# Kernel optimization log

Measured on AMD Instinct MI355X. Metric: run time of the kernel, lower is better.

## Reference

```python
import jax, jax.numpy as jnp
import numpy as np

B, LC, LQ = 16, 512, 64
H = 256            # args.hidden_dim (BiLSTM output dim)
D = 4 * H          # feedforward / biaffine input dim
DFF = 512          # args.hidden_dim_ffw
C = 3              # num_labels


def setup_inputs() -> dict:
    key = jax.random.key(0)
    ks = jax.random.split(key, 12)
    sc = 0.02
    return {
        "ctx_emb": jax.random.normal(ks[0], (B, LC, H), jnp.float32),
        "ques_emb": jax.random.normal(ks[1], (B, LQ, H), jnp.float32),
        "w_sim": jax.random.normal(ks[2], (3 * H,), jnp.float32) * sc,
        "W1s": jax.random.normal(ks[3], (D, DFF), jnp.float32) * sc,
        "b1s": jnp.zeros((DFF,), jnp.float32),
        "W2s": jax.random.normal(ks[4], (DFF, D), jnp.float32) * sc,
        "b2s": jnp.zeros((D,), jnp.float32),
        "W1e": jax.random.normal(ks[5], (D, DFF), jnp.float32) * sc,
        "b1e": jnp.zeros((DFF,), jnp.float32),
        "W2e": jax.random.normal(ks[6], (DFF, D), jnp.float32) * sc,
        "b2e": jnp.zeros((D,), jnp.float32),
        "Wb": jax.random.normal(ks[7], (D + 1, C, D + 1), jnp.float32) * sc,
    }


def _ffw(x, W1, b1, W2, b2):
    # FeedforwardLayer: w_2(relu(w_1(x))) (dropout is identity at eval)
    return jnp.maximum(x @ W1 + b1, 0.0) @ W2 + b2


def reference(ctx_emb, ques_emb, w_sim, W1s, b1s, W2s, b2s, W1e, b1e, W2e, b2e, Wb):
    w1, w2, w3 = jnp.split(w_sim, 3)
    # Fused BiDAF trilinear similarity: identical math to
    # Linear(cat([ctx_, ques_, ctx_*ques_], -1)) with weight [w1|w2|w3].
    sim = (ctx_emb @ w1)[:, :, None] + (ques_emb @ w2)[:, None, :] \
        + jnp.einsum('bih,bjh->bij', ctx_emb * w3, ques_emb)      # [B,LC,LQ]
    a = jax.nn.softmax(sim, axis=-1)                               # [B,LC,LQ]
    c2q = jnp.einsum('bij,bjh->bih', a, ques_emb)                  # [B,LC,H]
    b = jax.nn.softmax(jnp.max(sim, axis=2), axis=-1)              # [B,LC]
    q2c = jnp.einsum('bi,bih->bh', b, ctx_emb)[:, None, :]         # [B,1,H] broadcast over LC
    x = jnp.concatenate([ctx_emb, c2q, ctx_emb * c2q, ctx_emb * q2c], axis=2)  # [B,LC,4H]
    start = _ffw(x, W1s, b1s, W2s, b2s)                            # [B,LC,D]
    end = _ffw(x, W1e, b1e, W2e, b2e)                              # [B,LC,D]
    ones = jnp.ones(start.shape[:-1] + (1,), start.dtype)
    s1 = jnp.concatenate([start, ones], axis=-1)                   # [B,LC,D+1]
    e1 = jnp.concatenate([end, ones], axis=-1)                     # [B,LC,D+1]
    # Biaffine: score[b,x,y,c] = s1[b,x] . Wb[:,c,:] . e1[b,y]
    return jnp.einsum('bxi,icj,byj->bxyc', s1, Wb, e1)             # [B,LC,LC,C]
```

## Files before the change

kernel.cpp:

```cpp
#include <hip/hip_runtime.h>
#include <hip/hip_bf16.h>
#include <math.h>

typedef __bf16 bf16_t;
typedef bf16_t bf16x4 __attribute__((ext_vector_type(4)));
typedef bf16_t bf16x8 __attribute__((ext_vector_type(8)));
typedef float f32x4 __attribute__((ext_vector_type(4)));

#define Bsz 16
#define LCc 512
#define LQq 64
#define Hd 256
#define Dd 1024
#define DFFd 512
#define DP1 1025
#define KP 1152
#define NTT 18
#define NROW 8192
#define YC 1536

#define OFF_T    0L
#define OFF_QW2  0L
#define OFF_MROW 4096L
#define OFF_Q2C  36864L
#define OFF_C2Q  53248L
#define OFF_XB   8441856L
#define OFF_HBUF 25219072L
#define OFF_W1C  41996288L
#define OFF_W2C  44093440L
#define OFF_S1   56623104L
#define OFF_E1   75497472L
#define OFF_WBT  94371840L

static __device__ __forceinline__ void gload_lds16(const void* g, void* l) {
    __builtin_amdgcn_global_load_lds(
        (const __attribute__((address_space(1))) void*)g,
        (__attribute__((address_space(3))) void*)l, 16, 0, 0);
}

__global__ __launch_bounds__(256) void k_qw2(const float* __restrict__ ques,
                                             const float* __restrict__ wsim,
                                             float* __restrict__ qw2) {
    int row = blockIdx.x * 4 + (threadIdx.x >> 6);
    int lane = threadIdx.x & 63;
    float4 q = *(const float4*)&ques[(long)row * Hd + lane * 4];
    float4 w = *(const float4*)&wsim[Hd + lane * 4];
    float p = q.x * w.x + q.y * w.y + q.z * w.z + q.w * w.w;
#pragma unroll
    for (int o = 32; o >= 1; o >>= 1) p += __shfl_xor(p, o, 64);
    if (lane == 0) qw2[row] = p;
}

__global__ __launch_bounds__(256) void k_wtrans(const float* __restrict__ in,
                                                bf16_t* __restrict__ out,
                                                int K, int N) {
    __shared__ float tile[32][33];
    int k0 = blockIdx.x * 32, n0 = blockIdx.y * 32;
    int r = threadIdx.x >> 5, c = threadIdx.x & 31;
#pragma unroll
    for (int rr = 0; rr < 32; rr += 8)
        tile[r + rr][c] = in[(long)(k0 + r + rr) * N + n0 + c];
    __syncthreads();
#pragma unroll
    for (int rr = 0; rr < 32; rr += 8)
        out[(long)(n0 + r + rr) * K + k0 + c] = (bf16_t)tile[c][r + rr];
}

__global__ __launch_bounds__(256) void k_wb(const float* __restrict__ Wb,
                                            bf16_t* __restrict__ Wbt) {
    int rw = blockIdx.x;
    int c = rw >> 10, i = rw & 1023;
    int tid = threadIdx.x;
    const float* src = Wb + ((long)i * 3 + c) * DP1;
    bf16_t* orow = Wbt + (long)rw * KP;
#pragma unroll
    for (int p = 0; p < 2; p++) {
        int j4 = tid + p * 256;
        if (j4 < KP / 4) {
            int j = j4 * 4;
            float x = (j + 0 < DP1) ? src[j + 0] : 0.f;
            float y = (j + 1 < DP1) ? src[j + 1] : 0.f;
            float z = (j + 2 < DP1) ? src[j + 2] : 0.f;
            float w = (j + 3 < DP1) ? src[j + 3] : 0.f;
            bf16x4 bv = {(bf16_t)x, (bf16_t)y, (bf16_t)z, (bf16_t)w};
            *(bf16x4*)&orow[j] = bv;
        }
    }
}

__global__ __launch_bounds__(256) void k_initse(bf16_t* __restrict__ s1,
                                                bf16_t* __restrict__ e1) {
    int idx = blockIdx.x * 256 + threadIdx.x;
    long r = idx >> 7; int cc = idx & 127;
    bf16_t v = (bf16_t)(cc == 0 ? 1.0f : 0.0f);
    s1[r * KP + 1024 + cc] = v;
    e1[r * KP + 1024 + cc] = v;
}

__global__ __launch_bounds__(256) void k_attn(const float* __restrict__ ctx,
                                              const float* __restrict__ ques,
                                              const float* __restrict__ wsim,
                                              const float* __restrict__ qw2,
                                              float* __restrict__ c2q,
                                              float* __restrict__ mrow) {
    __shared__ bf16x4 qlds[LQq * 64];
    __shared__ float cw3s[4][Hd];
    __shared__ float awave[4][LQq];
    int b = blockIdx.x >> 5;
    int itile = blockIdx.x & 31;
    int tid = threadIdx.x, wid = tid >> 6, lane = tid & 63;
#pragma unroll
    for (int p = 0; p < 16; p++) {
        int s = tid + p * 256;
        int j = s >> 6, h4s = s & 63;
        int h4 = h4s ^ (j & 15);
        float4 v = *(const float4*)&ques[((long)b * LQq + j) * Hd + h4 * 4];
        bf16x4 bv = {(bf16_t)v.x, (bf16_t)v.y, (bf16_t)v.z, (bf16_t)v.w};
        qlds[s] = bv;
    }
    float qw2r = qw2[b * LQq + lane];
    float4 w1v = *(const float4*)&wsim[lane * 4];
    float4 w3v = *(const float4*)&wsim[2 * Hd + lane * 4];
    __syncthreads();
    for (int rr = 0; rr < 4; rr++) {
        int i = itile * 16 + wid * 4 + rr;
        float4 cv = *(const float4*)&ctx[((long)b * LCc + i) * Hd + lane * 4];
        float cw1p = cv.x * w1v.x + cv.y * w1v.y + cv.z * w1v.z + cv.w * w1v.w;
        float4 c3;
        c3.x = cv.x * w3v.x; c3.y = cv.y * w3v.y;
        c3.z = cv.z * w3v.z; c3.w = cv.w * w3v.w;
        *(float4*)&cw3s[wid][lane * 4] = c3;
#pragma unroll
        for (int o = 32; o >= 1; o >>= 1) cw1p += __shfl_xor(cw1p, o, 64);
        __syncthreads();
        float s = cw1p + qw2r;
#pragma unroll 8
        for (int h4 = 0; h4 < 64; h4++) {
            float4 c3v = *(const float4*)&cw3s[wid][h4 * 4];
            bf16x4 qb = qlds[lane * 64 + (h4 ^ (lane & 15))];
            s += c3v.x * (float)qb[0] + c3v.y * (float)qb[1]
               + c3v.z * (float)qb[2] + c3v.w * (float)qb[3];
        }
        float mx = s;
#pragma unroll
        for (int o = 32; o >= 1; o >>= 1) mx = fmaxf(mx, __shfl_xor(mx, o, 64));
        if (lane == 0) mrow[b * LCc + i] = mx;
        float pe = __expf(s - mx);
        float den = pe;
#pragma unroll
        for (int o = 32; o >= 1; o >>= 1) den += __shfl_xor(den, o, 64);
        awave[wid][lane] = pe / den;
        __syncthreads();
        float4 accv = {0.f, 0.f, 0.f, 0.f};
#pragma unroll 8
        for (int j = 0; j < 64; j++) {
            float aj = awave[wid][j];
            bf16x4 qb = qlds[j * 64 + (lane ^ (j & 15))];
            accv.x = fmaf(aj, (float)qb[0], accv.x);
            accv.y = fmaf(aj, (float)qb[1], accv.y);
            accv.z = fmaf(aj, (float)qb[2], accv.z);
            accv.w = fmaf(aj, (float)qb[3], accv.w);
        }
        *(float4*)&c2q[((long)b * LCc + i) * Hd + lane * 4] = accv;
        __syncthreads();
    }
}

__global__ __launch_bounds__(256) void k_q2c(const float* __restrict__ ctx,
                                             const float* __restrict__ mrow,
                                             float* __restrict__ q2c) {
    __shared__ float wbuf[LCc];
    __shared__ float red[8];
    __shared__ float part[8][32];
    int blk = blockIdx.x;
    int b = blk >> 3, hc = blk & 7;
    int tid = threadIdx.x;
    float v0 = mrow[b * LCc + tid], v1 = mrow[b * LCc + 256 + tid];
    float m = fmaxf(v0, v1);
#pragma unroll
    for (int o = 32; o >= 1; o >>= 1) m = fmaxf(m, __shfl_xor(m, o, 64));
    if ((tid & 63) == 0) red[tid >> 6] = m;
    __syncthreads();
    float M = fmaxf(fmaxf(red[0], red[1]), fmaxf(red[2], red[3]));
    float e0 = __expf(v0 - M), e1v = __expf(v1 - M);
    float sm = e0 + e1v;
#pragma unroll
    for (int o = 32; o >= 1; o >>= 1) sm += __shfl_xor(sm, o, 64);
    if ((tid & 63) == 0) red[4 + (tid >> 6)] = sm;
    __syncthreads();
    float S = red[4] + red[5] + red[6] + red[7];
    wbuf[tid] = e0 / S;
    wbuf[tid + 256] = e1v / S;
    __syncthreads();
    int ig = tid >> 5, h31 = tid & 31;
    int h = hc * 32 + h31;
    float acc = 0.f;
#pragma unroll 4
    for (int ii = 0; ii < 64; ii++) {
        int i = ig * 64 + ii;
        acc = fmaf(wbuf[i], ctx[((long)b * LCc + i) * Hd + h], acc);
    }
    part[ig][h31] = acc;
    __syncthreads();
    if (tid < 32) {
        float s = 0.f;
#pragma unroll
        for (int k = 0; k < 8; k++) s += part[k][tid];
        q2c[b * Hd + hc * 32 + tid] = s;
    }
}

__global__ __launch_bounds__(256) void k_buildx(const float* __restrict__ ctx,
                                                const float* __restrict__ c2q,
                                                const float* __restrict__ q2c,
                                                bf16_t* __restrict__ xb) {
    long r = blockIdx.x;
    int b = (int)(r >> 9);
    int tid = threadIdx.x;
    int sec = tid >> 6, h4 = tid & 63;
    float4 cv = *(const float4*)&ctx[r * Hd + h4 * 4];
    float4 v;
    if (sec == 0) {
        v = cv;
    } else if (sec == 1) {
        v = *(const float4*)&c2q[r * Hd + h4 * 4];
    } else if (sec == 2) {
        float4 q = *(const float4*)&c2q[r * Hd + h4 * 4];
        v.x = cv.x * q.x; v.y = cv.y * q.y; v.z = cv.z * q.z; v.w = cv.w * q.w;
    } else {
        float4 q = *(const float4*)&q2c[b * Hd + h4 * 4];
        v.x = cv.x * q.x; v.y = cv.y * q.y; v.z = cv.z * q.z; v.w = cv.w * q.w;
    }
    bf16x4 bv = {(bf16_t)v.x, (bf16_t)v.y, (bf16_t)v.z, (bf16_t)v.w};
    *(bf16x4*)&xb[r * Dd + sec * Hd + h4 * 4] = bv;
}

__global__ __launch_bounds__(256) void k_gcol(const bf16_t* __restrict__ e1,
                                              const float* __restrict__ Wb,
                                              bf16_t* __restrict__ T) {
    int tid = threadIdx.x;
    int wv = tid >> 6, lane = tid & 63;
    long r = (long)blockIdx.x * 4 + wv;
    bf16x8 ea = *(const bf16x8*)&e1[r * KP + lane * 16];
    bf16x8 eb = *(const bf16x8*)&e1[r * KP + lane * 16 + 8];
    const float* wr0 = Wb + (long)3072 * DP1;
#pragma unroll
    for (int c = 0; c < 3; c++) {
        const float* wr = wr0 + (long)c * DP1 + lane * 16;
        float acc = 0.f;
#pragma unroll
        for (int k = 0; k < 8; k++) {
            acc = fmaf((float)ea[k], wr[k], acc);
            acc = fmaf((float)eb[k], wr[8 + k], acc);
        }
#pragma unroll
        for (int o = 32; o >= 1; o >>= 1) acc += __shfl_xor(acc, o, 64);
        long rowb = (r * 3 + c) * (long)KP;
        if (lane == 0)
            T[rowb + 1024] = (bf16_t)(acc + wr0[(long)c * DP1 + 1024]);
        for (int jj = 1025 + lane; jj < KP; jj += 64)
            T[rowb + jj] = (bf16_t)0.f;
    }
}

template <int MODE>
__global__ __launch_bounds__(256, 2) void gemm_nt(
    const bf16_t* __restrict__ A, const bf16_t* __restrict__ B,
    const float* __restrict__ bias0, const float* __restrict__ bias1,
    bf16_t* __restrict__ C0, bf16_t* __restrict__ C1) {
    const int K = (MODE == 0) ? 1024 : 512;
    const int lda = 1024;
    const int ldb = (MODE == 0) ? 1024 : 512;
    __shared__ bf16_t As[128 * 32];
    __shared__ bf16_t Bs[128 * 32];
    int tid = threadIdx.x;
    int wid = tid >> 6, lane = tid & 63;
    int z = (MODE == 1) ? blockIdx.z : 0;
    const bf16_t* Ab = A + (long)blockIdx.x * 128 * lda + z * 512;
    const bf16_t* Bb = B + (long)z * 1024 * 512 + (long)blockIdx.y * 128 * ldb;
    int wr = (wid >> 1) * 64, wc = (wid & 1) * 64;
    int fr = lane & 15, kg = lane >> 4;
    f32x4 acc[4][4] = {};
    for (int k0 = 0; k0 < K; k0 += 32) {
        __syncthreads();
#pragma unroll
        for (int p = 0; p < 2; p++) {
            int q = tid + p * 256;
            int row = q >> 2, cg = q & 3;
            gload_lds16(Ab + (long)row * lda + k0 + cg * 8, &As[q * 8]);
            gload_lds16(Bb + (long)row * ldb + k0 + cg * 8, &Bs[q * 8]);
        }
        __syncthreads();
        bf16x8 af[4], bq[4];
#pragma unroll
        for (int m = 0; m < 4; m++)
            af[m] = *(const bf16x8*)&As[(wr + m * 16 + fr) * 32 + kg * 8];
#pragma unroll
        for (int n = 0; n < 4; n++)
            bq[n] = *(const bf16x8*)&Bs[(wc + n * 16 + fr) * 32 + kg * 8];
#pragma unroll
        for (int m = 0; m < 4; m++)
#pragma unroll
            for (int n = 0; n < 4; n++)
                acc[m][n] = __builtin_amdgcn_mfma_f32_16x16x32_bf16(
                    af[m], bq[n], acc[m][n], 0, 0, 0);
    }
    int g4 = (lane >> 4) * 4;
#pragma unroll
    for (int m = 0; m < 4; m++) {
#pragma unroll
        for (int g = 0; g < 4; g++) {
            long r = (long)blockIdx.x * 128 + wr + m * 16 + g4 + g;
#pragma unroll
            for (int n = 0; n < 4; n++) {
                int col = blockIdx.y * 128 + wc + n * 16 + fr;
                float v = acc[m][n][g];
                if (MODE == 0) {
                    v += (col < 512) ? bias0[col] : bias1[col - 512];
                    v = fmaxf(v, 0.f);
                    C0[r * 1024 + col] = (bf16_t)v;
                } else {
                    v += z ? bias1[col] : bias0[col];
                    (z ? C1 : C0)[r * (long)KP + col] = (bf16_t)v;
                }
            }
        }
    }
}

template <int MODE>
__global__ __launch_bounds__(512) void gemm8(
    const bf16_t* __restrict__ A, const bf16_t* __restrict__ B,
    void* __restrict__ C) {
    __shared__ char smem[131072];
    int tid = threadIdx.x;
    int wg = blockIdx.x;
    int bx, zz, yy;
    if (MODE == 2) {
        int wgid = (wg & 7) * 48 + (wg >> 3);
        int wi = wgid & 15, st = wgid >> 4;
        bx = (st & 7) * 4 + (wi & 3);
        int byN = (st >> 3) * 4 + (wi >> 2);
        zz = byN >> 2; yy = byN & 3;
    } else {
        int wgid = (wg & 7) * 24 + (wg >> 3);
        bx = wgid & 1;
        int byz = wgid >> 1;
        zz = byz / 6; yy = byz % 6;
    }
    long Aoff = (MODE == 2) ? (long)bx * 256 * KP
                            : ((long)zz * 512 + bx * 256) * KP;
    long Boff = (MODE == 2) ? (long)(zz * 4 + yy) * 256 * KP
                            : ((long)zz * 1536 + yy * 256) * KP;
    const bf16_t* At = A + Aoff;
    const bf16_t* Bt = B + Boff;
    int lane = tid & 63, wv = tid >> 6, wm = wv >> 2, wn = wv & 3;
    int fr = lane & 15, kg = lane >> 4;
    int row0 = tid >> 3, sc0 = (tid & 7) ^ (row0 & 7);
    int q1 = tid + 512;
    int row1 = q1 >> 3, sc1 = (q1 & 7) ^ (row1 & 7);

    auto STAGE = [&](int mat, int ht, int tile) {
        int ts = tile <= NTT - 1 ? tile : NTT - 1;
        int buf = tile & 1;
        const bf16_t* base = mat ? Bt : At;
        long rb = (long)ht * 128;
        const bf16_t* g0 = base + (rb + row0) * KP + ts * 64 + sc0 * 8;
        const bf16_t* g1 = base + (rb + row1) * KP + ts * 64 + sc1 * 8;
        char* l = smem + (mat ? 65536 : 0) + buf * 32768 + ht * 16384;
        gload_lds16(g0, l + tid * 16);
        gload_lds16(g1, l + 8192 + tid * 16);
    };
    auto RDA = [&](int buf, int h, int m, int kk) -> bf16x8 {
        int row = wm * 128 + h * 64 + m * 16 + fr;
        int c16 = kk * 4 + kg;
        int off = buf * 32768 + row * 128 + ((c16 ^ (row & 7)) << 4);
        return *(const bf16x8*)(smem + off);
    };
    auto RDB = [&](int buf, int v, int n, int kk) -> bf16x8 {
        int row = wn * 64 + v * 32 + n * 16 + fr;
        int c16 = kk * 4 + kg;
        int off = 65536 + buf * 32768 + row * 128 + ((c16 ^ (row & 7)) << 4);
        return *(const bf16x8*)(smem + off);
    };

    f32x4 acc[8][4] = {};

    STAGE(0, 0, 0); STAGE(0, 1, 0); STAGE(1, 0, 0); STAGE(1, 1, 0);
    STAGE(0, 0, 1); STAGE(0, 1, 1);
    asm volatile("s_waitcnt vmcnt(4)" ::: "memory");
    __builtin_amdgcn_s_barrier();

    auto doTile = [&](int buf, int sB, int sA) {
        bf16x8 aL[4][2], aH[4][2], bE[2][2], bO[2][2];
#pragma unroll
        for (int m = 0; m < 4; m++)
#pragma unroll
            for (int k = 0; k < 2; k++) aL[m][k] = RDA(buf, 0, m, k);
#pragma unroll
        for (int n = 0; n < 2; n++)
#pragma unroll
            for (int k = 0; k < 2; k++) bE[n][k] = RDB(buf, 0, n, k);
        STAGE(1, 0, sB);
        __builtin_amdgcn_s_barrier();
        __builtin_amdgcn_s_setprio(1);
#pragma unroll
        for (int m = 0; m < 4; m++)
#pragma unroll
            for (int n = 0; n < 2; n++)
#pragma unroll
                for (int k = 0; k < 2; k++)
                    acc[m][n] = __builtin_amdgcn_mfma_f32_16x16x32_bf16(
                        aL[m][k], bE[n][k], acc[m][n], 0, 0, 0);
        __builtin_amdgcn_s_setprio(0);
        __builtin_amdgcn_s_barrier();
#pragma unroll
        for (int n = 0; n < 2; n++)
#pragma unroll
            for (int k = 0; k < 2; k++) bO[n][k] = RDB(buf, 1, n, k);
        STAGE(1, 1, sB);
        __builtin_amdgcn_s_barrier();
        __builtin_amdgcn_s_setprio(1);
#pragma unroll
        for (int m = 0; m < 4; m++)
#pragma unroll
            for (int n = 0; n < 2; n++)
#pragma unroll
                for (int k = 0; k < 2; k++)
                    acc[m][2 + n] = __builtin_amdgcn_mfma_f32_16x16x32_bf16(
                        aL[m][k], bO[n][k], acc[m][2 + n], 0, 0, 0);
        __builtin_amdgcn_s_setprio(0);
        __builtin_amdgcn_s_barrier();
#pragma unroll
        for (int m = 0; m < 4; m++)
#pragma unroll
            for (int k = 0; k < 2; k++) aH[m][k] = RDA(buf, 1, m, k);
        STAGE(0, 0, sA);
        __builtin_amdgcn_s_barrier();
        __builtin_amdgcn_s_setprio(1);
#pragma unroll
        for (int m = 0; m < 4; m++)
#pragma unroll
            for (int n = 0; n < 2; n++)
#pragma unroll
                for (int k = 0; k < 2; k++)
                    acc[4 + m][n] = __builtin_amdgcn_mfma_f32_16x16x32_bf16(
                        aH[m][k], bE[n][k], acc[4 + m][n], 0, 0, 0);
        __builtin_amdgcn_s_setprio(0);
        __builtin_amdgcn_s_barrier();
        STAGE(0, 1, sA);
        __builtin_amdgcn_s_barrier();
        __builtin_amdgcn_s_setprio(1);
#pragma unroll
        for (int m = 0; m < 4; m++)
#pragma unroll
            for (int n = 0; n < 2; n++)
#pragma unroll
                for (int k = 0; k < 2; k++)
                    acc[4 + m][2 + n] = __builtin_amdgcn_mfma_f32_16x16x32_bf16(
                        aH[m][k], bO[n][k], acc[4 + m][2 + n], 0, 0, 0);
        __builtin_amdgcn_s_setprio(0);
        asm volatile("s_waitcnt vmcnt(4)" ::: "memory");
        __builtin_amdgcn_s_barrier();
    };

    for (int it = 0; it < NTT / 2; ++it) {
        int t = 2 * it;
        doTile(0, t + 1, t + 2);
        doTile(1, t + 2, t + 3);
    }

#pragma unroll
    for (int mf = 0; mf < 8; mf++) {
#pragma unroll
        for (int g = 0; g < 4; g++) {
            int rloc = wm * 128 + mf * 16 + kg * 4 + g;
#pragma unroll
            for (int nf = 0; nf < 4; nf++) {
                int col = wn * 64 + nf * 16 + fr;
                float v = acc[mf][nf][g];
                if (MODE == 2) {
                    long r = (long)bx * 256 + rloc;
                    ((bf16_t*)C)[(r * 3 + zz) * (long)KP + yy * 256 + col] = (bf16_t)v;
                } else {
                    long r = (long)bx * 256 + rloc;
                    ((float*)C)[(long)zz * (512L * YC) + r * YC + yy * 256 + col] = v;
                }
            }
        }
    }
}

extern "C" void kernel_launch(void* const* d_in, const int* in_sizes, int n_in,
                              void* d_out, int out_size, void* d_ws, size_t ws_size,
                              hipStream_t stream) {
    const float* ctx  = (const float*)d_in[0];
    const float* ques = (const float*)d_in[1];
    const float* wsim = (const float*)d_in[2];
    const float* W1s  = (const float*)d_in[3];
    const float* b1s  = (const float*)d_in[4];
    const float* W2s  = (const float*)d_in[5];
    const float* b2s  = (const float*)d_in[6];
    const float* W1e  = (const float*)d_in[7];
    const float* b1e  = (const float*)d_in[8];
    const float* W2e  = (const float*)d_in[9];
    const float* b2e  = (const float*)d_in[10];
    const float* Wb   = (const float*)d_in[11];

    char* ws = (char*)d_ws;
    float*  qw2  = (float*)(ws + OFF_QW2);
    float*  mrow = (float*)(ws + OFF_MROW);
    float*  q2c  = (float*)(ws + OFF_Q2C);
    float*  c2q  = (float*)(ws + OFF_C2Q);
    bf16_t* xb   = (bf16_t*)(ws + OFF_XB);
    bf16_t* hbuf = (bf16_t*)(ws + OFF_HBUF);
    bf16_t* W1c  = (bf16_t*)(ws + OFF_W1C);
    bf16_t* W2c  = (bf16_t*)(ws + OFF_W2C);
    bf16_t* T    = (bf16_t*)(ws + OFF_T);
    bf16_t* s1   = (bf16_t*)(ws + OFF_S1);
    bf16_t* e1   = (bf16_t*)(ws + OFF_E1);
    bf16_t* Wbt  = (bf16_t*)(ws + OFF_WBT);

    k_qw2<<<256, 256, 0, stream>>>(ques, wsim, qw2);
    k_wtrans<<<dim3(32, 16), 256, 0, stream>>>(W1s, W1c, 1024, 512);
    k_wtrans<<<dim3(32, 16), 256, 0, stream>>>(W1e, W1c + 512 * 1024, 1024, 512);
    k_wtrans<<<dim3(16, 32), 256, 0, stream>>>(W2s, W2c, 512, 1024);
    k_wtrans<<<dim3(16, 32), 256, 0, stream>>>(W2e, W2c + 1024 * 512, 512, 1024);
    k_wb<<<3072, 256, 0, stream>>>(Wb, Wbt);
    k_attn<<<Bsz * 32, 256, 0, stream>>>(ctx, ques, wsim, qw2, c2q, mrow);
    k_q2c<<<128, 256, 0, stream>>>(ctx, mrow, q2c);
    k_buildx<<<NROW, 256, 0, stream>>>(ctx, c2q, q2c, xb);
    k_initse<<<4096, 256, 0, stream>>>(s1, e1);

    gemm_nt<0><<<dim3(64, 8), 256, 0, stream>>>(xb, W1c, b1s, b1e, hbuf, nullptr);
    gemm_nt<1><<<dim3(64, 8, 2), 256, 0, stream>>>(hbuf, W2c, b2s, b2e, s1, e1);
    k_gcol<<<2048, 256, 0, stream>>>(e1, Wb, T);
    gemm8<2><<<384, 512, 0, stream>>>(e1, Wbt, T);
    gemm8<3><<<192, 512, 0, stream>>>(s1, T, d_out);
}
```

Baseline: 314.7 us.

## Generalize 8-wave pipelined GEMM and use it for feedforward and biaffine stages

Replaces the simple 128x128 single-buffered feedforward GEMMs with a templated 8-wave, double-buffered, swizzled-LDS GEMM whose N-fragment count and K-tile count are template parameters. The biaffine GEMMs are retiled from 256-wide to 192-wide N tiles, with XCD-aware block mapping to raise grid size and balance work across CUs. The four weight-transpose launches are merged into two using a z grid dimension. The cost is more LDS per block and more complex index math, with possible occupancy or register pressure changes.

```diff
diff --git a/kernel.cpp b/kernel.cpp
--- a/kernel.cpp
+++ b/kernel.cpp
@@ -15,7 +15,6 @@
 #define DFFd 512
 #define DP1 1025
 #define KP 1152
-#define NTT 18
 #define NROW 8192
 #define YC 1536
 
@@ -51,10 +50,13 @@
     if (lane == 0) qw2[row] = p;
 }
 
-__global__ __launch_bounds__(256) void k_wtrans(const float* __restrict__ in,
-                                                bf16_t* __restrict__ out,
-                                                int K, int N) {
+__global__ __launch_bounds__(256) void k_wtrans2(const float* __restrict__ in0,
+                                                 const float* __restrict__ in1,
+                                                 bf16_t* __restrict__ out,
+                                                 int K, int N) {
     __shared__ float tile[32][33];
+    const float* in = blockIdx.z ? in1 : in0;
+    bf16_t* o = out + (long)blockIdx.z * K * N;
     int k0 = blockIdx.x * 32, n0 = blockIdx.y * 32;
     int r = threadIdx.x >> 5, c = threadIdx.x & 31;
 #pragma unroll
@@ -63,7 +65,7 @@
     __syncthreads();
 #pragma unroll
     for (int rr = 0; rr < 32; rr += 8)
-        out[(long)(n0 + r + rr) * K + k0 + c] = (bf16_t)tile[c][r + rr];
+        o[(long)(n0 + r + rr) * K + k0 + c] = (bf16_t)tile[c][r + rr];
 }
 
 __global__ __launch_bounds__(256) void k_wb(const float* __restrict__ Wb,
@@ -263,113 +265,64 @@
     }
 }
 
-template <int MODE>
-__global__ __launch_bounds__(256, 2) void gemm_nt(
+template <int NT, int NFR, int MODE>
+__global__ __launch_bounds__(512) void gemm8p(
     const bf16_t* __restrict__ A, const bf16_t* __restrict__ B,
-    const float* __restrict__ bias0, const float* __restrict__ bias1,
-    bf16_t* __restrict__ C0, bf16_t* __restrict__ C1) {
-    const int K = (MODE == 0) ? 1024 : 512;
-    const int lda = 1024;
-    const int ldb = (MODE == 0) ? 1024 : 512;
-    __shared__ bf16_t As[128 * 32];
-    __shared__ bf16_t Bs[128 * 32];
-    int tid = threadIdx.x;
-    int wid = tid >> 6, lane = tid & 63;
-    int z = (MODE == 1) ? blockIdx.z : 0;
-    const bf16_t* Ab = A + (long)blockIdx.x * 128 * lda + z * 512;
-    const bf16_t* Bb = B + (long)z * 1024 * 512 + (long)blockIdx.y * 128 * ldb;
-    int wr = (wid >> 1) * 64, wc = (wid & 1) * 64;
-    int fr = lane & 15, kg = lane >> 4;
-    f32x4 acc[4][4] = {};
-    for (int k0 = 0; k0 < K; k0 += 32) {
-        __syncthreads();
-#pragma unroll
-        for (int p = 0; p < 2; p++) {
-            int q = tid + p * 256;
-            int row = q >> 2, cg = q & 3;
-            gload_lds16(Ab + (long)row * lda + k0 + cg * 8, &As[q * 8]);
-            gload_lds16(Bb + (long)row * ldb + k0 + cg * 8, &Bs[q * 8]);
-        }
-        __syncthreads();
-        bf16x8 af[4], bq[4];
-#pragma unroll
-        for (int m = 0; m < 4; m++)
-            af[m] = *(const bf16x8*)&As[(wr + m * 16 + fr) * 32 + kg * 8];
-#pragma unroll
-        for (int n = 0; n < 4; n++)
-            bq[n] = *(const bf16x8*)&Bs[(wc + n * 16 + fr) * 32 + kg * 8];
-#pragma unroll
-        for (int m = 0; m < 4; m++)
-#pragma unroll
-            for (int n = 0; n < 4; n++)
-                acc[m][n] = __builtin_amdgcn_mfma_f32_16x16x32_bf16(
-                    af[m], bq[n], acc[m][n], 0, 0, 0);
-    }
-    int g4 = (lane >> 4) * 4;
-#pragma unroll
-    for (int m = 0; m < 4; m++) {
-#pragma unroll
-        for (int g = 0; g < 4; g++) {
-            long r = (long)blockIdx.x * 128 + wr + m * 16 + g4 + g;
-#pragma unroll
-            for (int n = 0; n < 4; n++) {
-                int col = blockIdx.y * 128 + wc + n * 16 + fr;
-                float v = acc[m][n][g];
-                if (MODE == 0) {
-                    v += (col < 512) ? bias0[col] : bias1[col - 512];
-                    v = fmaxf(v, 0.f);
-                    C0[r * 1024 + col] = (bf16_t)v;
-                } else {
-                    v += z ? bias1[col] : bias0[col];
-                    (z ? C1 : C0)[r * (long)KP + col] = (bf16_t)v;
-                }
-            }
-        }
-    }
-}
-
-template <int MODE>
-__global__ __launch_bounds__(512) void gemm8(
-    const bf16_t* __restrict__ A, const bf16_t* __restrict__ B,
-    void* __restrict__ C) {
-    __shared__ char smem[131072];
+    const float* __restrict__ b0, const float* __restrict__ b1,
+    void* __restrict__ C0, void* __restrict__ C1) {
+    constexpr int LDA = (MODE <= 1) ? 1024 : KP;
+    constexpr int LDB = (MODE == 0) ? 1024 : (MODE == 1) ? 512 : KP;
+    constexpr int BEn = (NFR + 1) / 2;
+    constexpr int BOn = NFR / 2;
+    __shared__ char smem[65536 + NFR * 16384];
     int tid = threadIdx.x;
     int wg = blockIdx.x;
-    int bx, zz, yy;
-    if (MODE == 2) {
-        int wgid = (wg & 7) * 48 + (wg >> 3);
-        int wi = wgid & 15, st = wgid >> 4;
-        bx = (st & 7) * 4 + (wi & 3);
-        int byN = (st >> 3) * 4 + (wi >> 2);
-        zz = byN >> 2; yy = byN & 3;
+    int xcd = wg & 7, idx = wg >> 3;
+    int bx, by, z = 0;
+    if (MODE == 0) {
+        bx = (xcd & 3) * 8 + (idx & 7); by = (xcd >> 2) * 4 + (idx >> 3);
+    } else if (MODE == 1) {
+        z = idx >> 4; bx = (xcd & 3) * 8 + (idx & 7); by = (xcd >> 2) * 2 + ((idx >> 3) & 1);
+    } else if (MODE == 2) {
+        bx = (xcd & 3) * 8 + (idx & 7); by = (xcd >> 2) * 8 + (idx >> 3);
     } else {
-        int wgid = (wg & 7) * 24 + (wg >> 3);
-        bx = wgid & 1;
-        int byz = wgid >> 1;
-        zz = byz / 6; yy = byz % 6;
-    }
-    long Aoff = (MODE == 2) ? (long)bx * 256 * KP
-                            : ((long)zz * 512 + bx * 256) * KP;
-    long Boff = (MODE == 2) ? (long)(zz * 4 + yy) * 256 * KP
-                            : ((long)zz * 1536 + yy * 256) * KP;
-    const bf16_t* At = A + Aoff;
-    const bf16_t* Bt = B + Boff;
+        z = xcd * 2 + (idx >> 4); bx = idx & 1; by = (idx >> 1) & 7;
+    }
+    const bf16_t* At;
+    const bf16_t* Bt;
+    if (MODE == 0) {
+        At = A + (long)bx * 256 * LDA;            Bt = B + (long)by * 128 * LDB;
+    } else if (MODE == 1) {
+        At = A + (long)z * 512 + (long)bx * 256 * LDA;
+        Bt = B + (long)z * 524288 + (long)by * 256 * LDB;
+    } else if (MODE == 2) {
+        At = A + (long)bx * 256 * LDA;            Bt = B + (long)by * 192 * LDB;
+    } else {
+        At = A + ((long)z * 512 + bx * 256) * LDA;
+        Bt = B + ((long)z * 1536 + by * 192) * LDB;
+    }
     int lane = tid & 63, wv = tid >> 6, wm = wv >> 2, wn = wv & 3;
     int fr = lane & 15, kg = lane >> 4;
     int row0 = tid >> 3, sc0 = (tid & 7) ^ (row0 & 7);
     int q1 = tid + 512;
     int row1 = q1 >> 3, sc1 = (q1 & 7) ^ (row1 & 7);
 
-    auto STAGE = [&](int mat, int ht, int tile) {
-        int ts = tile <= NTT - 1 ? tile : NTT - 1;
+    auto stageA = [&](int half, int tile) {
+        int ts = tile <= NT - 1 ? tile : NT - 1;
         int buf = tile & 1;
-        const bf16_t* base = mat ? Bt : At;
-        long rb = (long)ht * 128;
-        const bf16_t* g0 = base + (rb + row0) * KP + ts * 64 + sc0 * 8;
-        const bf16_t* g1 = base + (rb + row1) * KP + ts * 64 + sc1 * 8;
-        char* l = smem + (mat ? 65536 : 0) + buf * 32768 + ht * 16384;
+        long rb = (long)half * 128;
+        const bf16_t* g0 = At + (rb + row0) * LDA + ts * 64 + sc0 * 8;
+        const bf16_t* g1 = At + (rb + row1) * LDA + ts * 64 + sc1 * 8;
+        char* l = smem + buf * 32768 + half * 16384;
         gload_lds16(g0, l + tid * 16);
         gload_lds16(g1, l + 8192 + tid * 16);
+    };
+    auto stageB = [&](int j, int tile) {
+        int ts = tile <= NT - 1 ? tile : NT - 1;
+        int buf = tile & 1;
+        const bf16_t* g0 = Bt + (long)(j * 64 + row0) * LDB + ts * 64 + sc0 * 8;
+        char* l = smem + 65536 + buf * (NFR * 8192) + j * 8192;
+        gload_lds16(g0, l + tid * 16);
     };
     auto RDA = [&](int buf, int h, int m, int kk) -> bf16x8 {
         int row = wm * 128 + h * 64 + m * 16 + fr;
@@ -377,37 +330,40 @@
         int off = buf * 32768 + row * 128 + ((c16 ^ (row & 7)) << 4);
         return *(const bf16x8*)(smem + off);
     };
-    auto RDB = [&](int buf, int v, int n, int kk) -> bf16x8 {
-        int row = wn * 64 + v * 32 + n * 16 + fr;
+    auto RDB = [&](int buf, int n, int kk) -> bf16x8 {
+        int row = wn * (16 * NFR) + n * 16 + fr;
         int c16 = kk * 4 + kg;
-        int off = 65536 + buf * 32768 + row * 128 + ((c16 ^ (row & 7)) << 4);
+        int off = 65536 + buf * (NFR * 8192) + row * 128 + ((c16 ^ (row & 7)) << 4);
         return *(const bf16x8*)(smem + off);
     };
 
-    f32x4 acc[8][4] = {};
-
-    STAGE(0, 0, 0); STAGE(0, 1, 0); STAGE(1, 0, 0); STAGE(1, 1, 0);
-    STAGE(0, 0, 1); STAGE(0, 1, 1);
+    f32x4 acc[8][NFR] = {};
+
+    stageA(0, 0); stageA(1, 0);
+#pragma unroll
+    for (int j = 0; j < NFR; j++) stageB(j, 0);
+    stageA(0, 1); stageA(1, 1);
     asm volatile("s_waitcnt vmcnt(4)" ::: "memory");
     __builtin_amdgcn_s_barrier();
 
     auto doTile = [&](int buf, int sB, int sA) {
-        bf16x8 aL[4][2], aH[4][2], bE[2][2], bO[2][2];
+        bf16x8 aL[4][2], aH[4][2], bE[BEn][2], bO[BOn][2];
 #pragma unroll
         for (int m = 0; m < 4; m++)
 #pragma unroll
             for (int k = 0; k < 2; k++) aL[m][k] = RDA(buf, 0, m, k);
 #pragma unroll
-        for (int n = 0; n < 2; n++)
-#pragma unroll
-            for (int k = 0; k < 2; k++) bE[n][k] = RDB(buf, 0, n, k);
-        STAGE(1, 0, sB);
+        for (int n = 0; n < BEn; n++)
+#pragma unroll
+            for (int k = 0; k < 2; k++) bE[n][k] = RDB(buf, n, k);
+#pragma unroll
+        for (int j = 0; j < BEn; j++) stageB(j, sB);
         __builtin_amdgcn_s_barrier();
         __builtin_amdgcn_s_setprio(1);
 #pragma unroll
         for (int m = 0; m < 4; m++)
 #pragma unroll
-            for (int n = 0; n < 2; n++)
+            for (int n = 0; n < BEn; n++)
 #pragma unroll
                 for (int k = 0; k < 2; k++)
                     acc[m][n] = __builtin_amdgcn_mfma_f32_16x16x32_bf16(
@@ -415,56 +371,57 @@
         __builtin_amdgcn_s_setprio(0);
         __builtin_amdgcn_s_barrier();
 #pragma unroll
-        for (int n = 0; n < 2; n++)
-#pragma unroll
-            for (int k = 0; k < 2; k++) bO[n][k] = RDB(buf, 1, n, k);
-        STAGE(1, 1, sB);
+        for (int n = 0; n < BOn; n++)
+#pragma unroll
+            for (int k = 0; k < 2; k++) bO[n][k] = RDB(buf, BEn + n, k);
+#pragma unroll
+        for (int j = BEn; j < NFR; j++) stageB(j, sB);
         __builtin_amdgcn_s_barrier();
         __builtin_amdgcn_s_setprio(1);
 #pragma unroll
         for (int m = 0; m < 4; m++)
 #pragma unroll
-            for (int n = 0; n < 2; n++)
+            for (int n = 0; n < BOn; n++)
 #pragma unroll
                 for (int k = 0; k < 2; k++)
-                    acc[m][2 + n] = __builtin_amdgcn_mfma_f32_16x16x32_bf16(
-                        aL[m][k], bO[n][k], acc[m][2 + n], 0, 0, 0);
+                    acc[m][BEn + n] = __builtin_amdgcn_mfma_f32_16x16x32_bf16(
+                        aL[m][k], bO[n][k], acc[m][BEn + n], 0, 0, 0);
         __builtin_amdgcn_s_setprio(0);
         __builtin_amdgcn_s_barrier();
 #pragma unroll
         for (int m = 0; m < 4; m++)
 #pragma unroll
             for (int k = 0; k < 2; k++) aH[m][k] = RDA(buf, 1, m, k);
-        STAGE(0, 0, sA);
+        stageA(0, sA);
         __builtin_amdgcn_s_barrier();
         __builtin_amdgcn_s_setprio(1);
 #pragma unroll
         for (int m = 0; m < 4; m++)
 #pragma unroll
-            for (int n = 0; n < 2; n++)
+            for (int n = 0; n < BEn; n++)
 #pragma unroll
                 for (int k = 0; k < 2; k++)
                     acc[4 + m][n] = __builtin_amdgcn_mfma_f32_16x16x32_bf16(
                         aH[m][k], bE[n][k], acc[4 + m][n], 0, 0, 0);
         __builtin_amdgcn_s_setprio(0);
         __builtin_amdgcn_s_barrier();
-        STAGE(0, 1, sA);
+        stageA(1, sA);
         __builtin_amdgcn_s_barrier();
         __builtin_amdgcn_s_setprio(1);
 #pragma unroll
         for (int m = 0; m < 4; m++)
 #pragma unroll
-            for (int n = 0; n < 2; n++)
+            for (int n = 0; n < BOn; n++)
 #pragma unroll
                 for (int k = 0; k < 2; k++)
-                    acc[4 + m][2 + n] = __builtin_amdgcn_mfma_f32_16x16x32_bf16(
-                        aH[m][k], bO[n][k], acc[4 + m][2 + n], 0, 0, 0);
+                    acc[4 + m][BEn + n] = __builtin_amdgcn_mfma_f32_16x16x32_bf16(
+                        aH[m][k], bO[n][k], acc[4 + m][BEn + n], 0, 0, 0);
         __builtin_amdgcn_s_setprio(0);
         asm volatile("s_waitcnt vmcnt(4)" ::: "memory");
         __builtin_amdgcn_s_barrier();
     };
 
-    for (int it = 0; it < NTT / 2; ++it) {
+    for (int it = 0; it < NT / 2; ++it) {
         int t = 2 * it;
         doTile(0, t + 1, t + 2);
         doTile(1, t + 2, t + 3);
@@ -475,16 +432,27 @@
 #pragma unroll
         for (int g = 0; g < 4; g++) {
             int rloc = wm * 128 + mf * 16 + kg * 4 + g;
-#pragma unroll
-            for (int nf = 0; nf < 4; nf++) {
-                int col = wn * 64 + nf * 16 + fr;
+            long r = (long)bx * 256 + rloc;
+#pragma unroll
+            for (int nf = 0; nf < NFR; nf++) {
+                int col = wn * (16 * NFR) + nf * 16 + fr;
                 float v = acc[mf][nf][g];
-                if (MODE == 2) {
-                    long r = (long)bx * 256 + rloc;
-                    ((bf16_t*)C)[(r * 3 + zz) * (long)KP + yy * 256 + col] = (bf16_t)v;
+                if (MODE == 0) {
+                    int colg = by * 128 + col;
+                    v += (colg < 512) ? b0[colg] : b1[colg - 512];
+                    v = fmaxf(v, 0.f);
+                    ((bf16_t*)C0)[r * 1024 + colg] = (bf16_t)v;
+                } else if (MODE == 1) {
+                    int colg = by * 256 + col;
+                    v += z ? b1[colg] : b0[colg];
+                    ((bf16_t*)(z ? C1 : C0))[r * (long)KP + colg] = (bf16_t)v;
+                } else if (MODE == 2) {
+                    int colg = by * 192 + col;
+                    int cls = colg >> 10, i = colg & 1023;
+                    ((bf16_t*)C0)[(r * 3 + cls) * (long)KP + i] = (bf16_t)v;
                 } else {
-                    long r = (long)bx * 256 + rloc;
-                    ((float*)C)[(long)zz * (512L * YC) + r * YC + yy * 256 + col] = v;
+                    int colg = by * 192 + col;
+                    ((float*)C0)[(long)z * (512L * YC) + r * YC + colg] = v;
                 }
             }
         }
@@ -522,19 +490,17 @@
     bf16_t* Wbt  = (bf16_t*)(ws + OFF_WBT);
 
     k_qw2<<<256, 256, 0, stream>>>(ques, wsim, qw2);
-    k_wtrans<<<dim3(32, 16), 256, 0, stream>>>(W1s, W1c, 1024, 512);
-    k_wtrans<<<dim3(32, 16), 256, 0, stream>>>(W1e, W1c + 512 * 1024, 1024, 512);
-    k_wtrans<<<dim3(16, 32), 256, 0, stream>>>(W2s, W2c, 512, 1024);
-    k_wtrans<<<dim3(16, 32), 256, 0, stream>>>(W2e, W2c + 1024 * 512, 512, 1024);
+    k_wtrans2<<<dim3(32, 16, 2), 256, 0, stream>>>(W1s, W1e, W1c, 1024, 512);
+    k_wtrans2<<<dim3(16, 32, 2), 256, 0, stream>>>(W2s, W2e, W2c, 512, 1024);
     k_wb<<<3072, 256, 0, stream>>>(Wb, Wbt);
     k_attn<<<Bsz * 32, 256, 0, stream>>>(ctx, ques, wsim, qw2, c2q, mrow);
     k_q2c<<<128, 256, 0, stream>>>(ctx, mrow, q2c);
     k_buildx<<<NROW, 256, 0, stream>>>(ctx, c2q, q2c, xb);
     k_initse<<<4096, 256, 0, stream>>>(s1, e1);
 
-    gemm_nt<0><<<dim3(64, 8), 256, 0, stream>>>(xb, W1c, b1s, b1e, hbuf, nullptr);
-    gemm_nt<1><<<dim3(64, 8, 2), 256, 0, stream>>>(hbuf, W2c, b2s, b2e, s1, e1);
+    gemm8p<16, 2, 0><<<256, 512, 0, stream>>>(xb, W1c, b1s, b1e, hbuf, nullptr);
+    gemm8p<8, 4, 1><<<256, 512, 0, stream>>>(hbuf, W2c, b2s, b2e, s1, e1);
     k_gcol<<<2048, 256, 0, stream>>>(e1, Wb, T);
-    gemm8<2><<<384, 512, 0, stream>>>(e1, Wbt, T);
-    gemm8<3><<<192, 512, 0, stream>>>(s1, T, d_out);
-}
+    gemm8p<18, 3, 2><<<512, 512, 0, stream>>>(e1, Wbt, nullptr, nullptr, T, nullptr);
+    gemm8p<18, 3, 3><<<256, 512, 0, stream>>>(s1, T, nullptr, nullptr, d_out, nullptr);
+}
```

Measured after the change: 298.4 us. -5.2%, faster.
